# Optimization experiments

Hardware: AMD Instinct MI355X
Metric: run time of the kernel (lower is better)

Reference implementation:

```python
import jax, jax.numpy as jnp
import numpy as np

N, E = 50000, 800000
IN, HID, HEADS = 64, 32, 4


def setup_inputs() -> dict:
    key = jax.random.key(0)
    ks = jax.random.split(key, 18)
    x = jax.random.normal(ks[0], (N, IN), jnp.float32)
    edge_index = jax.random.randint(ks[1], (2, E), 0, N)

    def lin(k, fan_in, fan_out):
        kw, kb = jax.random.split(k)
        bound = 1.0 / np.sqrt(fan_in)
        W = jax.random.uniform(kw, (fan_in, fan_out), jnp.float32, -bound, bound)
        b = jax.random.uniform(kb, (fan_out,), jnp.float32, -bound, bound)
        return W, b

    # layer 1: in=IN, out=HID per head, heads=HEADS, concat=True -> out dim HID*HEADS
    Wq1, bq1 = lin(ks[2], IN, HEADS * HID)
    Wk1, bk1 = lin(ks[3], IN, HEADS * HID)
    Wv1, bv1 = lin(ks[4], IN, HEADS * HID)
    Ws1, bs1 = lin(ks[5], IN, HEADS * HID)  # root/skip lin
    # layer 2: in=HID*HEADS, out=HID, heads=1, concat=False
    IN2 = HID * HEADS
    Wq2, bq2 = lin(ks[6], IN2, HID)
    Wk2, bk2 = lin(ks[7], IN2, HID)
    Wv2, bv2 = lin(ks[8], IN2, HID)
    Ws2, bs2 = lin(ks[9], IN2, HID)
    return dict(x=x, edge_index=edge_index,
                Wq1=Wq1, bq1=bq1, Wk1=Wk1, bk1=bk1, Wv1=Wv1, bv1=bv1, Ws1=Ws1, bs1=bs1,
                Wq2=Wq2, bq2=bq2, Wk2=Wk2, bk2=bk2, Wv2=Wv2, bv2=bv2, Ws2=Ws2, bs2=bs2)


def transformer_conv(x, src, dst, Wq, bq, Wk, bk, Wv, bv, Ws, bs, heads, out_ch, concat):
    """PyG TransformerConv (eval mode, root_weight=True, beta=False)."""
    n = x.shape[0]
    q = (x @ Wq + bq).reshape(n, heads, out_ch)  # [N,H,C]
    k = (x @ Wk + bk).reshape(n, heads, out_ch)
    v = (x @ Wv + bv).reshape(n, heads, out_ch)
    # per-edge attention logits: q_i . k_j / sqrt(C)
    logits = jnp.einsum('ehc,ehc->eh', q[dst], k[src]) / jnp.sqrt(jnp.float32(out_ch))
    # segment softmax over incoming edges of each target node
    m = jax.ops.segment_max(logits, dst, num_segments=n)          # [N,H]
    p = jnp.exp(logits - m[dst])                                   # [E,H]
    denom = jax.ops.segment_sum(p, dst, num_segments=n)            # [N,H]
    alpha = p / denom[dst]                                         # [E,H]
    agg = jax.ops.segment_sum(alpha[:, :, None] * v[src], dst, num_segments=n)  # [N,H,C]
    if concat:
        o = agg.reshape(n, heads * out_ch)
    else:
        o = agg.mean(axis=1)
    return o + x @ Ws + bs


def reference(x, edge_index,
              Wq1, bq1, Wk1, bk1, Wv1, bv1, Ws1, bs1,
              Wq2, bq2, Wk2, bk2, Wv2, bv2, Ws2, bs2):
    src, dst = edge_index[0], edge_index[1]
    h = transformer_conv(x, src, dst, Wq1, bq1, Wk1, bk1, Wv1, bv1, Ws1, bs1,
                         HEADS, HID, True)
    h = jax.nn.elu(h)
    out = transformer_conv(h, src, dst, Wq2, bq2, Wk2, bk2, Wv2, bv2, Ws2, bs2,
                           1, HID, False)
    return out
```

## Files before the change

### kernel.cpp

```cpp
#include <hip/hip_runtime.h>
#include <hip/hip_bf16.h>
#include <hip/hip_fp8.h>

#define N_NODES 50000
#define N_EDGES 800000
#define HB 3125
#define GB1 1563
#define NBS 49

static constexpr float SCALE = 0.17677669529663687f;

typedef __attribute__((ext_vector_type(8))) short bf16x8;
typedef __attribute__((ext_vector_type(4))) float f32x4;
typedef __attribute__((ext_vector_type(2))) float f32x2;
#define MFMA16 __builtin_amdgcn_mfma_f32_16x16x32_bf16
#define CVT8 __builtin_amdgcn_cvt_pk_f32_fp8

static __device__ inline unsigned short f2bf(float f) {
    __hip_bfloat16 h = __float2bfloat16(f);
    return __builtin_bit_cast(unsigned short, h);
}
static __device__ inline unsigned char f2fp8(float f) {
    __hip_fp8_e4m3 h(f);
    return __builtin_bit_cast(unsigned char, h);
}
static __device__ inline f32x2 bfp2(unsigned u) {
    f32x2 r;
    r[0] = __uint_as_float(u << 16);
    r[1] = __uint_as_float(u & 0xffff0000u);
    return r;
}
static __device__ inline bf16x8 cvt8(const float* p) {
    float4 f0 = *(const float4*)p;
    float4 f1 = *(const float4*)(p + 4);
    bf16x8 r;
    r[0] = (short)f2bf(f0.x); r[1] = (short)f2bf(f0.y);
    r[2] = (short)f2bf(f0.z); r[3] = (short)f2bf(f0.w);
    r[4] = (short)f2bf(f1.x); r[5] = (short)f2bf(f1.y);
    r[6] = (short)f2bf(f1.z); r[7] = (short)f2bf(f1.w);
    return r;
}


__global__ __launch_bounds__(256) void k_ph(
    const int* __restrict__ dst, int* __restrict__ cnt, int* __restrict__ rank,
    const float* __restrict__ Wq1, const float* __restrict__ Wk1,
    const float* __restrict__ Wv1, const float* __restrict__ Ws1,
    const float* __restrict__ Wq2, const float* __restrict__ Wk2,
    const float* __restrict__ Wv2, const float* __restrict__ Ws2,
    unsigned short* __restrict__ Wf1, unsigned short* __restrict__ Wf2)
{
    if (blockIdx.x < HB) {
        int e = blockIdx.x * 256 + threadIdx.x;
        rank[e] = atomicAdd(&cnt[dst[e]], 1);
        return;
    }
    int id = (blockIdx.x - HB) * 256 + threadIdx.x;
    if (id < 32768) {
        int j = id & 7, l = (id >> 3) & 63, ks = (id >> 9) & 1, nt = (id >> 10) & 7, m = (id >> 13) & 3;
        const float* W = (m == 0) ? Wq1 : (m == 1) ? Wk1 : (m == 2) ? Wv1 : Ws1;
        int k = ks * 32 + ((l >> 4) << 3) + j;
        int c = nt * 16 + (l & 15);
        Wf1[id] = f2bf(W[k * 128 + c]);
    } else if (id < 49152) {
        int id2 = id - 32768;
        int j = id2 & 7, l = (id2 >> 3) & 63, ks = (id2 >> 9) & 3, g = (id2 >> 11) & 7;
        int m = g >> 1, t = g & 1;
        const float* W = (m == 0) ? Wq2 : (m == 1) ? Wk2 : (m == 2) ? Wv2 : Ws2;
        int k = ks * 32 + ((l >> 4) << 3) + j;
        int c = t * 16 + (l & 15);
        Wf2[id2] = f2bf(W[k * 32 + c]);
    }
}


__global__ __launch_bounds__(256) void k_gs(
    const int* __restrict__ cnt, int* __restrict__ row, int* __restrict__ bsum,
    int* __restrict__ boff, int* __restrict__ ctr,
    const float* __restrict__ x, const unsigned short* __restrict__ Wf1,
    const float* __restrict__ bq, const float* __restrict__ bk,
    const float* __restrict__ bv, const float* __restrict__ bs,
    unsigned short* __restrict__ qs1, unsigned char* __restrict__ kv8, int n)
{
    __shared__ unsigned char smem[4 * 4352];
    if (blockIdx.x >= GB1) {
        __shared__ int wsum[4];
        __shared__ int lastBlk;
        int b = blockIdx.x - GB1;
        int t = threadIdx.x;
        int base = b * 1024 + t * 4;
        int v0 = (base + 0 < n) ? cnt[base + 0] : 0;
        int v1i = (base + 1 < n) ? cnt[base + 1] : 0;
        int v2 = (base + 2 < n) ? cnt[base + 2] : 0;
        int v3 = (base + 3 < n) ? cnt[base + 3] : 0;
        int s = v0 + v1i + v2 + v3;
        int lane = t & 63, wid = t >> 6;
        int sc = s;
#pragma unroll
        for (int d = 1; d < 64; d <<= 1) {
            int o = __shfl_up(sc, d);
            if (lane >= d) sc += o;
        }
        if (lane == 63) wsum[wid] = sc;
        __syncthreads();
        int woff = 0;
        for (int w = 0; w < wid; ++w) woff += wsum[w];
        int excl = woff + sc - s;
        if (base + 0 < n) row[base + 0] = excl;
        if (base + 1 < n) row[base + 1] = excl + v0;
        if (base + 2 < n) row[base + 2] = excl + v0 + v1i;
        if (base + 3 < n) row[base + 3] = excl + v0 + v1i + v2;
        if (t == 255) {
            bsum[b] = woff + sc;
            __threadfence();
            lastBlk = (atomicAdd(ctr, 1) == NBS - 1);
        }
        __syncthreads();
        if (lastBlk && t < 64) {
            __threadfence();
            int v = (t < NBS) ? ((volatile int*)bsum)[t] : 0;
            int sc2 = v;
#pragma unroll
            for (int d = 1; d < 64; d <<= 1) {
                int o = __shfl_up(sc2, d);
                if (t >= d) sc2 += o;
            }
            boff[t] = sc2 - v;
            if (t == (N_NODES >> 10)) row[N_NODES] = N_EDGES - (sc2 - v);
        }
        return;
    }
    int w = threadIdx.x >> 6;
    int l = threadIdx.x & 63;
    int rb = blockIdx.x * 32;
    int lr = l & 15, lk = l >> 4;
    f32x4 acc[2][8];
#pragma unroll
    for (int mt = 0; mt < 2; ++mt)
#pragma unroll
        for (int nt = 0; nt < 8; ++nt) acc[mt][nt] = (f32x4){0.f, 0.f, 0.f, 0.f};
#pragma unroll
    for (int ks = 0; ks < 2; ++ks) {
        bf16x8 a[2];
#pragma unroll
        for (int mt = 0; mt < 2; ++mt) {
            int r = rb + mt * 16 + lr;
            if (r >= n) r = n - 1;
            a[mt] = cvt8(x + (size_t)r * 64 + ks * 32 + lk * 8);
        }
#pragma unroll
        for (int nt = 0; nt < 8; ++nt) {
            bf16x8 b = *(const bf16x8*)(Wf1 + (size_t)((w * 8 + nt) * 1024 + ks * 512 + l * 8));
            acc[0][nt] = MFMA16(a[0], b, acc[0][nt], 0, 0, 0);
            acc[1][nt] = MFMA16(a[1], b, acc[1][nt], 0, 0, 0);
        }
    }
    const float* bptr = (w == 0) ? bq : (w == 1) ? bk : (w == 2) ? bv : bs;
    unsigned char* my = smem + w * 4352;
#pragma unroll
    for (int mt = 0; mt < 2; ++mt) {
        if (w == 1 || w == 2) {
            unsigned char* lb = my;
#pragma unroll
            for (int nt = 0; nt < 8; ++nt) {
                float bias = bptr[nt * 16 + lr];
#pragma unroll
                for (int i = 0; i < 4; ++i)
                    lb[(lk * 4 + i) * 144 + nt * 16 + lr] = f2fp8(acc[mt][nt][i] + bias);
            }
            int voff = (w == 2) ? 8 : 0;
#pragma unroll
            for (int p = 0; p < 4; ++p) {
                int rl = p * 4 + lk;
                int r = rb + mt * 16 + rl;
                if (r < n) {
                    uint2 val = *(const uint2*)(lb + rl * 144 + lr * 8);
                    *(uint2*)(kv8 + (size_t)r * 256 + lr * 16 + voff) = val;
                }
            }
        } else {
            unsigned short* ls = (unsigned short*)my;
#pragma unroll
            for (int nt = 0; nt < 8; ++nt) {
                float bias = bptr[nt * 16 + lr];
#pragma unroll
                for (int i = 0; i < 4; ++i)
                    ls[(lk * 4 + i) * 136 + nt * 16 + lr] = f2bf(acc[mt][nt][i] + bias);
            }
            unsigned short* outp = (w == 0) ? qs1 : qs1 + 128;
#pragma unroll
            for (int p = 0; p < 4; ++p) {
                int rl = p * 4 + lk;
                int r = rb + mt * 16 + rl;
                if (r < n) {
                    uint4 val = *(const uint4*)(ls + rl * 136 + lr * 8);
                    *(uint4*)(outp + (size_t)r * 256 + lr * 8) = val;
                }
            }
        }
    }
}


__global__ void k_scat(const int* __restrict__ src, const int* __restrict__ dst,
                       const int* __restrict__ row, const int* __restrict__ boff,
                       const int* __restrict__ rank, int* __restrict__ col) {
    int e = blockIdx.x * 256 + threadIdx.x;
    int de = dst[e];
    col[row[de] + boff[de >> 10] + rank[e]] = src[e];
}


__global__ __launch_bounds__(256) void k_gemm2m(
    const unsigned short* __restrict__ h1b, const unsigned short* __restrict__ Wf2,
    const float* __restrict__ bq, const float* __restrict__ bk,
    const float* __restrict__ bv, const float* __restrict__ bs,
    unsigned short* __restrict__ qs2, unsigned short* __restrict__ kv2, int n)
{
    __shared__ unsigned short lds[4][32][72];
    int w = threadIdx.x >> 6;
    int l = threadIdx.x & 63;
    int half = w & 1;
    int rb = blockIdx.x * 64 + (w >> 1) * 32;
    int lr = l & 15, lk = l >> 4;
    f32x4 acc[2][4];
#pragma unroll
    for (int mt = 0; mt < 2; ++mt)
#pragma unroll
        for (int nt = 0; nt < 4; ++nt) acc[mt][nt] = (f32x4){0.f, 0.f, 0.f, 0.f};
#pragma unroll
    for (int ks = 0; ks < 4; ++ks) {
        bf16x8 a[2];
#pragma unroll
        for (int mt = 0; mt < 2; ++mt) {
            int r = rb + mt * 16 + lr;
            if (r >= n) r = n - 1;
            a[mt] = *(const bf16x8*)(h1b + (size_t)r * 128 + ks * 32 + lk * 8);
        }
#pragma unroll
        for (int nt = 0; nt < 4; ++nt) {
            int g = half * 4 + nt;
            bf16x8 b = *(const bf16x8*)(Wf2 + (size_t)((g * 4 + ks) * 512 + l * 8));
            acc[0][nt] = MFMA16(a[0], b, acc[0][nt], 0, 0, 0);
            acc[1][nt] = MFMA16(a[1], b, acc[1][nt], 0, 0, 0);
        }
    }
#pragma unroll
    for (int nt = 0; nt < 4; ++nt) {
        int g = half * 4 + nt;
        int mat = g >> 1;
        int c = (g * 16 + lr) & 31;
        const float* bp = (mat == 0) ? bq : (mat == 1) ? bk : (mat == 2) ? bv : bs;
        float bias = bp[c];
#pragma unroll
        for (int mt = 0; mt < 2; ++mt)
#pragma unroll
            for (int i = 0; i < 4; ++i)
                lds[w][mt * 16 + lk * 4 + i][nt * 16 + lr] = f2bf(acc[mt][nt][i] + bias);
    }
    unsigned short* outA = (half == 0) ? qs2 : kv2 + 32;
    unsigned short* outB = (half == 0) ? kv2 : qs2 + 32;
    int rl8 = l >> 3, ci = (l & 7) * 4;
#pragma unroll
    for (int p = 0; p < 4; ++p) {
        int rl = p * 8 + rl8;
        int r = rb + rl;
        if (r < n) {
            uint2 va = *(const uint2*)&lds[w][rl][ci];
            *(uint2*)(outA + (size_t)r * 64 + ci) = va;
            uint2 vb = *(const uint2*)&lds[w][rl][32 + ci];
            *(uint2*)(outB + (size_t)r * 64 + ci) = vb;
        }
    }
}


__global__ __launch_bounds__(256) void k_agg1(
    const unsigned short* __restrict__ qs1, const unsigned char* __restrict__ kv8,
    const int* __restrict__ row, const int* __restrict__ boff,
    const int* __restrict__ col, uint4* __restrict__ h1b, int n)
{
    int i = blockIdx.x * 4 + (threadIdx.x >> 6);
    if (i >= n) return;
    int lane = threadIdx.x & 63;
    int slot = lane >> 4, w = lane & 15;
    f32x2 q2[4];
    {
        uint4 qu = *(const uint4*)(qs1 + (size_t)i * 256 + w * 8);
        q2[0] = bfp2(qu.x); q2[1] = bfp2(qu.y); q2[2] = bfp2(qu.z); q2[3] = bfp2(qu.w);
    }
    f32x2 acc2[4] = {};
    float d = 0.f;
    int s = row[i] + boff[i >> 10];
    int e = row[i + 1] + boff[(i + 1) >> 10];
    for (int t = s; t < e; t += 8) {
        int ta = t + slot, tb = t + 4 + slot;
        bool va = ta < e, vb = tb < e;
        int ja = col[va ? ta : s];
        int jb = col[vb ? tb : s];
        uint4 A = *(const uint4*)(kv8 + (size_t)ja * 256 + w * 16);
        uint4 B = *(const uint4*)(kv8 + (size_t)jb * 256 + w * 16);
        f32x2 pa = CVT8(A.x, false) * q2[0];
        pa += CVT8(A.x, true)  * q2[1];
        pa += CVT8(A.y, false) * q2[2];
        pa += CVT8(A.y, true)  * q2[3];
        f32x2 pb = CVT8(B.x, false) * q2[0];
        pb += CVT8(B.x, true)  * q2[1];
        pb += CVT8(B.y, false) * q2[2];
        pb += CVT8(B.y, true)  * q2[3];
        float la = pa[0] + pa[1];
        float lb = pb[0] + pb[1];
        la += __shfl_xor(la, 1);  lb += __shfl_xor(lb, 1);
        la += __shfl_xor(la, 2);  lb += __shfl_xor(lb, 2);
        float wa = va ? __expf(la * SCALE) : 0.f;
        float wb = vb ? __expf(lb * SCALE) : 0.f;
        d += wa + wb;
        f32x2 wa2 = (f32x2){wa, wa};
        f32x2 wb2 = (f32x2){wb, wb};
        acc2[0] += wa2 * CVT8(A.z, false);
        acc2[1] += wa2 * CVT8(A.z, true);
        acc2[2] += wa2 * CVT8(A.w, false);
        acc2[3] += wa2 * CVT8(A.w, true);
        acc2[0] += wb2 * CVT8(B.z, false);
        acc2[1] += wb2 * CVT8(B.z, true);
        acc2[2] += wb2 * CVT8(B.w, false);
        acc2[3] += wb2 * CVT8(B.w, true);
    }
    float acc[8] = {acc2[0][0], acc2[0][1], acc2[1][0], acc2[1][1],
                    acc2[2][0], acc2[2][1], acc2[3][0], acc2[3][1]};
#pragma unroll
    for (int m = 16; m <= 32; m <<= 1) {
        d += __shfl_xor(d, m);
#pragma unroll
        for (int c = 0; c < 8; ++c) acc[c] += __shfl_xor(acc[c], m);
    }
    if (slot == 0) {
        float inv = (d > 0.f) ? 1.f / d : 0.f;
        uint4 su = *(const uint4*)(qs1 + (size_t)i * 256 + 128 + w * 8);
        f32x2 sv[4] = {bfp2(su.x), bfp2(su.y), bfp2(su.z), bfp2(su.w)};
        unsigned o[4];
#pragma unroll
        for (int p = 0; p < 4; ++p) {
            float rx = acc[2 * p] * inv + sv[p][0];
            float ry = acc[2 * p + 1] * inv + sv[p][1];
            rx = (rx > 0.f) ? rx : expm1f(rx);
            ry = (ry > 0.f) ? ry : expm1f(ry);
            o[p] = ((unsigned)f2bf(ry) << 16) | (unsigned)f2bf(rx);
        }
        h1b[(size_t)i * 16 + w] = make_uint4(o[0], o[1], o[2], o[3]);
    }
}


__global__ __launch_bounds__(256) void k_agg2(
    const unsigned short* __restrict__ qs2, const unsigned short* __restrict__ kv2,
    const int* __restrict__ row, const int* __restrict__ boff,
    const int* __restrict__ col, float* __restrict__ out, int n)
{
    int i = blockIdx.x * 4 + (threadIdx.x >> 6);
    if (i >= n) return;
    int lane = threadIdx.x & 63;
    int slot = lane >> 2, qr = lane & 3;
    f32x2 q2[4];
    {
        uint4 qu = *(const uint4*)(qs2 + (size_t)i * 64 + qr * 8);
        q2[0] = bfp2(qu.x); q2[1] = bfp2(qu.y); q2[2] = bfp2(qu.z); q2[3] = bfp2(qu.w);
    }
    f32x2 acc2[4] = {};
    float d = 0.f;
    int s = row[i] + boff[i >> 10];
    int e = row[i + 1] + boff[(i + 1) >> 10];
    for (int t = s; t < e; t += 16) {
        int te = t + slot;
        bool va = te < e;
        int j = col[va ? te : s];
        const unsigned short* p = kv2 + (size_t)j * 64;
        uint4 ku = *(const uint4*)(p + qr * 8);
        uint4 vu = *(const uint4*)(p + 32 + qr * 8);
        f32x2 pp = bfp2(ku.x) * q2[0];
        pp += bfp2(ku.y) * q2[1];
        pp += bfp2(ku.z) * q2[2];
        pp += bfp2(ku.w) * q2[3];
        float lg = pp[0] + pp[1];
        lg += __shfl_xor(lg, 1);
        lg += __shfl_xor(lg, 2);
        float wv = va ? __expf(lg * SCALE) : 0.f;
        d += wv;
        f32x2 w2 = (f32x2){wv, wv};
        acc2[0] += w2 * bfp2(vu.x);
        acc2[1] += w2 * bfp2(vu.y);
        acc2[2] += w2 * bfp2(vu.z);
        acc2[3] += w2 * bfp2(vu.w);
    }
    float acc[8] = {acc2[0][0], acc2[0][1], acc2[1][0], acc2[1][1],
                    acc2[2][0], acc2[2][1], acc2[3][0], acc2[3][1]};
#pragma unroll
    for (int m = 4; m <= 32; m <<= 1) {
        d += __shfl_xor(d, m);
#pragma unroll
        for (int c = 0; c < 8; ++c) acc[c] += __shfl_xor(acc[c], m);
    }
    if (slot == 0) {
        float inv = (d > 0.f) ? 1.f / d : 0.f;
        uint4 su = *(const uint4*)(qs2 + (size_t)i * 64 + 32 + qr * 8);
        f32x2 sv[4] = {bfp2(su.x), bfp2(su.y), bfp2(su.z), bfp2(su.w)};
        float4 o0, o1;
        o0.x = acc[0] * inv + sv[0][0];
        o0.y = acc[1] * inv + sv[0][1];
        o0.z = acc[2] * inv + sv[1][0];
        o0.w = acc[3] * inv + sv[1][1];
        o1.x = acc[4] * inv + sv[2][0];
        o1.y = acc[5] * inv + sv[2][1];
        o1.z = acc[6] * inv + sv[3][0];
        o1.w = acc[7] * inv + sv[3][1];
        *(float4*)&out[(size_t)i * 32 + qr * 8] = o0;
        *(float4*)&out[(size_t)i * 32 + qr * 8 + 4] = o1;
    }
}


extern "C" void kernel_launch(void* const* d_in, const int* in_sizes, int n_in,
                              void* d_out, int out_size, void* d_ws, size_t ws_size,
                              hipStream_t stream)
{
    const int N = N_NODES, E = N_EDGES;
    const float* x   = (const float*)d_in[0];
    const int* edge  = (const int*)d_in[1];
    const int* src   = edge;
    const int* dst   = edge + E;
    const float* Wq1 = (const float*)d_in[2];  const float* bq1 = (const float*)d_in[3];
    const float* Wk1 = (const float*)d_in[4];  const float* bk1 = (const float*)d_in[5];
    const float* Wv1 = (const float*)d_in[6];  const float* bv1 = (const float*)d_in[7];
    const float* Ws1 = (const float*)d_in[8];  const float* bs1 = (const float*)d_in[9];
    const float* Wq2 = (const float*)d_in[10]; const float* bq2 = (const float*)d_in[11];
    const float* Wk2 = (const float*)d_in[12]; const float* bk2 = (const float*)d_in[13];
    const float* Wv2 = (const float*)d_in[14]; const float* bv2 = (const float*)d_in[15];
    const float* Ws2 = (const float*)d_in[16]; const float* bs2 = (const float*)d_in[17];

    char* ws = (char*)d_ws;
    size_t off = 0;
    auto alloc = [&](size_t bytes) -> void* {
        void* p = ws + off;
        off += (bytes + 255) & ~(size_t)255;
        return p;
    };
    unsigned short* qs1 = (unsigned short*)alloc((size_t)N * 256 * 2);
    unsigned char*  kv8 = (unsigned char*)alloc((size_t)N * 256);
    unsigned short* h1b = (unsigned short*)alloc((size_t)N * 128 * 2);
    unsigned short* qs2 = (unsigned short*)alloc((size_t)N * 64 * 2);
    unsigned short* kv2 = (unsigned short*)alloc((size_t)N * 64 * 2);
    unsigned short* Wf1 = (unsigned short*)alloc(32768 * 2);
    unsigned short* Wf2 = (unsigned short*)alloc(16384 * 2);
    int* row_ptr  = (int*)alloc((size_t)(N + 1) * 4);
    int* cnt      = (int*)alloc((size_t)(N + 64) * 4);
    int* ctr      = cnt + N;
    int* rank     = (int*)alloc((size_t)E * 4);
    int* colb     = (int*)alloc((size_t)E * 4);
    int* bsum     = (int*)alloc(64 * 4);
    int* boff     = (int*)alloc(64 * 4);

    hipMemsetAsync(cnt, 0, (size_t)(N + 64) * 4, stream);
    k_ph<<<HB + 192, 256, 0, stream>>>(dst, cnt, rank,
                                       Wq1, Wk1, Wv1, Ws1, Wq2, Wk2, Wv2, Ws2,
                                       Wf1, Wf2);
    k_gs<<<GB1 + NBS, 256, 0, stream>>>(cnt, row_ptr, bsum, boff, ctr,
                                        x, Wf1, bq1, bk1, bv1, bs1, qs1, kv8, N);
    k_scat<<<HB, 256, 0, stream>>>(src, dst, row_ptr, boff, rank, colb);
    k_agg1<<<(N + 3) / 4, 256, 0, stream>>>(qs1, kv8, row_ptr, boff, colb, (uint4*)h1b, N);
    k_gemm2m<<<(N + 63) / 64, 256, 0, stream>>>(h1b, Wf2, bq2, bk2, bv2, bs2, qs2, kv2, N);
    k_agg2<<<(N + 3) / 4, 256, 0, stream>>>(qs2, kv2, row_ptr, boff, colb, (float*)d_out, N);
}
```

Before: 163.8 us.

## Store layer-2 keys in FP8 and stage x through LDS in layer-1 GEMM

Layer-2 keys are now stored as FP8 in a separate 32-byte-per-node array and values in their own bf16 array. k_agg2 converts the keys with the packed FP8 conversion, which cuts the bytes gathered per edge from 128 to 96. Separately, the layer-1 GEMM converts each x tile to bf16 once into LDS, instead of every wave reloading and converting it from global memory. FP8 keys lower the precision of the attention logits. The LDS staging adds two block barriers and reuses the shared buffer that the epilogue also writes.

```diff
diff --git a/kernel.cpp b/kernel.cpp
--- a/kernel.cpp
+++ b/kernel.cpp
@@ -28,16 +28,6 @@
     f32x2 r;
     r[0] = __uint_as_float(u << 16);
     r[1] = __uint_as_float(u & 0xffff0000u);
-    return r;
-}
-static __device__ inline bf16x8 cvt8(const float* p) {
-    float4 f0 = *(const float4*)p;
-    float4 f1 = *(const float4*)(p + 4);
-    bf16x8 r;
-    r[0] = (short)f2bf(f0.x); r[1] = (short)f2bf(f0.y);
-    r[2] = (short)f2bf(f0.z); r[3] = (short)f2bf(f0.w);
-    r[4] = (short)f2bf(f1.x); r[5] = (short)f2bf(f1.y);
-    r[6] = (short)f2bf(f1.z); r[7] = (short)f2bf(f1.w);
     return r;
 }
 
@@ -134,6 +124,20 @@
     int l = threadIdx.x & 63;
     int rb = blockIdx.x * 32;
     int lr = l & 15, lk = l >> 4;
+    unsigned short* xs = (unsigned short*)smem;
+    {
+        int t = threadIdx.x;
+        int r = rb + (t >> 3);
+        if (r >= n) r = n - 1;
+        int c = (t & 7) * 8;
+        const float* xp = x + (size_t)r * 64 + c;
+        float4 f0 = *(const float4*)xp;
+        float4 f1 = *(const float4*)(xp + 4);
+        unsigned short* dp = xs + (t >> 3) * 72 + c;
+        dp[0] = f2bf(f0.x); dp[1] = f2bf(f0.y); dp[2] = f2bf(f0.z); dp[3] = f2bf(f0.w);
+        dp[4] = f2bf(f1.x); dp[5] = f2bf(f1.y); dp[6] = f2bf(f1.z); dp[7] = f2bf(f1.w);
+    }
+    __syncthreads();
     f32x4 acc[2][8];
 #pragma unroll
     for (int mt = 0; mt < 2; ++mt)
@@ -143,11 +147,8 @@
     for (int ks = 0; ks < 2; ++ks) {
         bf16x8 a[2];
 #pragma unroll
-        for (int mt = 0; mt < 2; ++mt) {
-            int r = rb + mt * 16 + lr;
-            if (r >= n) r = n - 1;
-            a[mt] = cvt8(x + (size_t)r * 64 + ks * 32 + lk * 8);
-        }
+        for (int mt = 0; mt < 2; ++mt)
+            a[mt] = *(const bf16x8*)(xs + (mt * 16 + lr) * 72 + ks * 32 + lk * 8);
 #pragma unroll
         for (int nt = 0; nt < 8; ++nt) {
             bf16x8 b = *(const bf16x8*)(Wf1 + (size_t)((w * 8 + nt) * 1024 + ks * 512 + l * 8));
@@ -155,6 +156,7 @@
             acc[1][nt] = MFMA16(a[1], b, acc[1][nt], 0, 0, 0);
         }
     }
+    __syncthreads();
     const float* bptr = (w == 0) ? bq : (w == 1) ? bk : (w == 2) ? bv : bs;
     unsigned char* my = smem + w * 4352;
 #pragma unroll
@@ -215,7 +217,8 @@
     const unsigned short* __restrict__ h1b, const unsigned short* __restrict__ Wf2,
     const float* __restrict__ bq, const float* __restrict__ bk,
     const float* __restrict__ bv, const float* __restrict__ bs,
-    unsigned short* __restrict__ qs2, unsigned short* __restrict__ kv2, int n)
+    unsigned short* __restrict__ qs2, unsigned char* __restrict__ k82,
+    unsigned short* __restrict__ v2, int n)
 {
     __shared__ unsigned short lds[4][32][72];
     int w = threadIdx.x >> 6;
@@ -258,8 +261,6 @@
             for (int i = 0; i < 4; ++i)
                 lds[w][mt * 16 + lk * 4 + i][nt * 16 + lr] = f2bf(acc[mt][nt][i] + bias);
     }
-    unsigned short* outA = (half == 0) ? qs2 : kv2 + 32;
-    unsigned short* outB = (half == 0) ? kv2 : qs2 + 32;
     int rl8 = l >> 3, ci = (l & 7) * 4;
 #pragma unroll
     for (int p = 0; p < 4; ++p) {
@@ -267,9 +268,19 @@
         int r = rb + rl;
         if (r < n) {
             uint2 va = *(const uint2*)&lds[w][rl][ci];
-            *(uint2*)(outA + (size_t)r * 64 + ci) = va;
             uint2 vb = *(const uint2*)&lds[w][rl][32 + ci];
-            *(uint2*)(outB + (size_t)r * 64 + ci) = vb;
+            if (half == 0) {
+                *(uint2*)(qs2 + (size_t)r * 64 + ci) = va;
+                unsigned pk =
+                      (unsigned)f2fp8(__uint_as_float(vb.x << 16))
+                    | ((unsigned)f2fp8(__uint_as_float(vb.x & 0xffff0000u)) << 8)
+                    | ((unsigned)f2fp8(__uint_as_float(vb.y << 16)) << 16)
+                    | ((unsigned)f2fp8(__uint_as_float(vb.y & 0xffff0000u)) << 24);
+                *(unsigned*)(k82 + (size_t)r * 32 + ci) = pk;
+            } else {
+                *(uint2*)(v2 + (size_t)r * 32 + ci) = va;
+                *(uint2*)(qs2 + (size_t)r * 64 + 32 + ci) = vb;
+            }
         }
     }
 }
@@ -353,7 +364,8 @@
 
 
 __global__ __launch_bounds__(256) void k_agg2(
-    const unsigned short* __restrict__ qs2, const unsigned short* __restrict__ kv2,
+    const unsigned short* __restrict__ qs2, const unsigned char* __restrict__ k82,
+    const unsigned short* __restrict__ v2,
     const int* __restrict__ row, const int* __restrict__ boff,
     const int* __restrict__ col, float* __restrict__ out, int n)
 {
@@ -374,13 +386,12 @@
         int te = t + slot;
         bool va = te < e;
         int j = col[va ? te : s];
-        const unsigned short* p = kv2 + (size_t)j * 64;
-        uint4 ku = *(const uint4*)(p + qr * 8);
-        uint4 vu = *(const uint4*)(p + 32 + qr * 8);
-        f32x2 pp = bfp2(ku.x) * q2[0];
-        pp += bfp2(ku.y) * q2[1];
-        pp += bfp2(ku.z) * q2[2];
-        pp += bfp2(ku.w) * q2[3];
+        uint2 ku = *(const uint2*)(k82 + (size_t)j * 32 + qr * 8);
+        uint4 vu = *(const uint4*)(v2 + (size_t)j * 32 + qr * 8);
+        f32x2 pp = CVT8(ku.x, false) * q2[0];
+        pp += CVT8(ku.x, true)  * q2[1];
+        pp += CVT8(ku.y, false) * q2[2];
+        pp += CVT8(ku.y, true)  * q2[3];
         float lg = pp[0] + pp[1];
         lg += __shfl_xor(lg, 1);
         lg += __shfl_xor(lg, 2);
@@ -448,7 +459,8 @@
     unsigned char*  kv8 = (unsigned char*)alloc((size_t)N * 256);
     unsigned short* h1b = (unsigned short*)alloc((size_t)N * 128 * 2);
     unsigned short* qs2 = (unsigned short*)alloc((size_t)N * 64 * 2);
-    unsigned short* kv2 = (unsigned short*)alloc((size_t)N * 64 * 2);
+    unsigned char*  k82 = (unsigned char*)alloc((size_t)N * 32);
+    unsigned short* v2  = (unsigned short*)alloc((size_t)N * 32 * 2);
     unsigned short* Wf1 = (unsigned short*)alloc(32768 * 2);
     unsigned short* Wf2 = (unsigned short*)alloc(16384 * 2);
     int* row_ptr  = (int*)alloc((size_t)(N + 1) * 4);
@@ -467,6 +479,6 @@
                                         x, Wf1, bq1, bk1, bv1, bs1, qs1, kv8, N);
     k_scat<<<HB, 256, 0, stream>>>(src, dst, row_ptr, boff, rank, colb);
     k_agg1<<<(N + 3) / 4, 256, 0, stream>>>(qs1, kv8, row_ptr, boff, colb, (uint4*)h1b, N);
-    k_gemm2m<<<(N + 63) / 64, 256, 0, stream>>>(h1b, Wf2, bq2, bk2, bv2, bs2, qs2, kv2, N);
-    k_agg2<<<(N + 3) / 4, 256, 0, stream>>>(qs2, kv2, row_ptr, boff, colb, (float*)d_out, N);
-}
+    k_gemm2m<<<(N + 63) / 64, 256, 0, stream>>>(h1b, Wf2, bq2, bk2, bv2, bs2, qs2, k82, v2, N);
+    k_agg2<<<(N + 3) / 4, 256, 0, stream>>>(qs2, k82, v2, row_ptr, boff, colb, (float*)d_out, N);
+}
```

New measurement: 157.2 us. -4.0%, faster.
